# Optimization experiments

Hardware: AMD Instinct MI355X
Metric: run time of the kernel (lower is better)

## Reference

```python
import jax, jax.numpy as jnp
import numpy as np


def _conv(x, w, b, s):
    # x: NCHW, w: OIHW, VALID padding, stride s
    y = jax.lax.conv_general_dilated(x, w, (s, s), 'VALID',
                                     dimension_numbers=('NCHW', 'OIHW', 'NCHW'))
    return y + b[None, :, None, None]


def _deconv(x, w, b, s):
    # PyTorch ConvTranspose2d (weight IOHW, padding=0): conv of input dilated by s
    # with spatially-flipped, in/out-swapped kernel and full padding k-1.
    k = w.shape[2]
    wk = jnp.flip(w, (2, 3)).transpose(1, 0, 2, 3)  # -> OIHW
    y = jax.lax.conv_general_dilated(x, wk, (1, 1), [(k - 1, k - 1), (k - 1, k - 1)],
                                     lhs_dilation=(s, s),
                                     dimension_numbers=('NCHW', 'OIHW', 'NCHW'))
    return y + b[None, :, None, None]


def setup_inputs() -> dict:
    key = jax.random.key(0)
    ks = iter(jax.random.split(key, 40))
    def p(shape, scale=0.05):
        return jax.random.normal(next(ks), shape, jnp.float32) * scale
    return dict(
        x=jax.random.normal(next(ks), (50, 1, 64, 64), jnp.float32),
        action=jax.random.normal(next(ks), (50, 30), jnp.float32),
        h0=jax.random.normal(next(ks), (50, 1024), jnp.float32),
        c0=jax.random.normal(next(ks), (50, 1024), jnp.float32),
        conv1_w=p((32, 1, 4, 4)), conv1_b=p((32,)),
        conv2_w=p((64, 32, 4, 4)), conv2_b=p((64,)),
        conv3_w=p((128, 64, 4, 4)), conv3_b=p((128,)),
        conv4_w=p((256, 128, 4, 4)), conv4_b=p((256,)),
        fc1_w=p((482, 1024)), fc1_b=p((482,)),
        fc2_w=p((1024, 512)), fc2_b=p((1024,)),
        w_ih=p((4096, 1024)), w_hh=p((4096, 1024)),
        b_ih=p((4096,)), b_hh=p((4096,)),
        fcsd_w=p((1024, 1024)), fcsd_b=p((1024,)),
        d1_w=p((1024, 128, 5, 5)), d1_b=p((128,)),
        d2_w=p((128, 64, 5, 5)), d2_b=p((64,)),
        d3_w=p((64, 32, 6, 6)), d3_b=p((32,)),
        d4_w=p((32, 1, 6, 6)), d4_b=p((1,)),
        fc5_w=p((1, 512)), fc5_b=p((1,)),
    )


def reference(x, action, h0, c0,
              conv1_w, conv1_b, conv2_w, conv2_b, conv3_w, conv3_b, conv4_w, conv4_b,
              fc1_w, fc1_b, fc2_w, fc2_b,
              w_ih, w_hh, b_ih, b_hh,
              fcsd_w, fcsd_b,
              d1_w, d1_b, d2_w, d2_b, d3_w, d3_b, d4_w, d4_b,
              fc5_w, fc5_b):
    B = x.shape[0]  # 50 (hardcoded in original)
    T = 17          # PHYRE_MAX_TIMESTEPS
    h = x
    for w, b in ((conv1_w, conv1_b), (conv2_w, conv2_b), (conv3_w, conv3_b), (conv4_w, conv4_b)):
        h = jnp.tanh(_conv(h, w, b, 2))
    flat = h.reshape(B, -1)                      # [50, 1024]
    fc1 = flat @ fc1_w.T + fc1_b                 # [50, 482]
    z = jnp.concatenate([fc1, action], axis=1)   # [50, 512]
    fc2_out = jax.nn.leaky_relu(z @ fc2_w.T + fc2_b)  # [50, 1024]

    def step(carry, _):
        xt, hs, cs = carry
        g = xt @ w_ih.T + b_ih + hs @ w_hh.T + b_hh   # [B, 4096], gates i,f,g,o
        i, f, gg, o = jnp.split(g, 4, axis=1)
        cs = jax.nn.sigmoid(f) * cs + jax.nn.sigmoid(i) * jnp.tanh(gg)
        hs = jax.nn.sigmoid(o) * jnp.tanh(cs)
        return (hs, hs, cs), hs  # output fed back as next input

    _, outs = jax.lax.scan(step, (fc2_out, h0, c0), None, length=T)  # [17, 50, 1024]
    hd = jax.nn.leaky_relu(jnp.einsum('tbd,ed->tbe', outs, fcsd_w) + fcsd_b)
    hd = hd.reshape(T * B, 1024, 1, 1)  # t-major flatten, matching torch .view
    y = jnp.tanh(_deconv(hd, d1_w, d1_b, 2))   # [850,128,5,5]
    y = jnp.tanh(_deconv(y, d2_w, d2_b, 2))    # [850,64,13,13]
    y = jnp.tanh(_deconv(y, d3_w, d3_b, 2))    # [850,32,30,30]
    y = _deconv(y, d4_w, d4_b, 2)              # [850,1,64,64]
    obs = y.reshape(B, T, 1, 64, 64)  # faithful to original's view (layout quirk)
    reward = z @ fc5_w.T + fc5_b      # [50, 1]
    return obs, reward
```

## Files before the change

kernel.cpp:

```cpp
#include <hip/hip_runtime.h>
#include <math.h>

#define DI __device__ __forceinline__

DI float sigm(float x){ return 1.0f/(1.0f+expf(-x)); }
DI float lrelu(float x){ return x > 0.f ? x : 0.01f*x; }

template<int ACT>
DI float act_apply(float v){
    if (ACT == 1) return tanhf(v);
    if (ACT == 2) return lrelu(v);
    return v;
}

template<int CIN, int COUT>
__global__ __launch_bounds__(256)
void conv_enc_kernel(const float* __restrict__ in, const float* __restrict__ w,
                     const float* __restrict__ bias, float* __restrict__ out,
                     int N, int H, int OH)
{
    int idx = blockIdx.x*256 + threadIdx.x;
    int total = N*COUT*OH*OH;
    if (idx >= total) return;
    int ox = idx % OH; int t = idx / OH;
    int oy = t % OH;   t /= OH;
    int o  = t % COUT; int n = t / COUT;
    float acc = bias[o];
    const float* wp = w + o*CIN*16;
    const float* ip = in + ((size_t)n*CIN)*H*H + (oy*2)*H + ox*2;
    for (int c = 0; c < CIN; ++c) {
        const float* ipc = ip + c*H*H;
        const float* wpc = wp + c*16;
        #pragma unroll
        for (int ky = 0; ky < 4; ++ky)
            #pragma unroll
            for (int kx = 0; kx < 4; ++kx)
                acc += ipc[ky*H + kx] * wpc[ky*4 + kx];
    }
    out[idx] = tanhf(acc);
}

template<int BM,int BN,int BK,bool BT,int ACT>
__global__ __launch_bounds__((BM/4)*(BN/4))
void gemm_kernel(const float* __restrict__ A, const float* __restrict__ Bm,
                 const float* __restrict__ bias, float* __restrict__ C,
                 int M, int N, int Kfull, int klen, int ldc, int bias_div,
                 long partStride)
{
    constexpr int TM = 4, TN = 4;
    constexpr int THREADS = (BM/TM)*(BN/TN);
    constexpr int LDA = BM + 4, LDB = BN + 4;
    __shared__ __align__(16) float As[BK][LDA];
    __shared__ __align__(16) float Bs[BK][LDB];
    int tid = threadIdx.x;
    int m0 = blockIdx.y * BM, n0 = blockIdx.x * BN;
    int koff = blockIdx.z * klen;
    C += (long)blockIdx.z * partStride;
    constexpr int NTX = BN/TN;
    int tx = tid % NTX, ty = tid / NTX;
    float acc[4][4];
    #pragma unroll
    for (int i=0;i<4;++i)
        #pragma unroll
        for (int j=0;j<4;++j) acc[i][j] = 0.f;

    for (int k0 = 0; k0 < klen; k0 += BK) {
        for (int e = tid; e < BM*BK; e += THREADS) {
            int k = e % BK, m = e / BK;
            As[k][m] = (m0+m < M) ? A[(size_t)(m0+m)*Kfull + koff + k0 + k] : 0.f;
        }
        if (BT) {
            for (int e = tid; e < BN*BK; e += THREADS) {
                int k = e % BK, n = e / BK;
                Bs[k][n] = (n0+n < N) ? Bm[(size_t)(n0+n)*Kfull + koff + k0 + k] : 0.f;
            }
        } else {
            for (int e = tid; e < BN*BK; e += THREADS) {
                int n = e % BN, k = e / BN;
                Bs[k][n] = (n0+n < N) ? Bm[(size_t)(koff + k0 + k)*N + n0+n] : 0.f;
            }
        }
        __syncthreads();
        #pragma unroll 8
        for (int k = 0; k < BK; ++k) {
            float4 a4 = *reinterpret_cast<const float4*>(&As[k][ty*4]);
            float4 b4 = *reinterpret_cast<const float4*>(&Bs[k][tx*4]);
            float av[4] = {a4.x, a4.y, a4.z, a4.w};
            float bv[4] = {b4.x, b4.y, b4.z, b4.w};
            #pragma unroll
            for (int i=0;i<4;++i)
                #pragma unroll
                for (int j=0;j<4;++j)
                    acc[i][j] += av[i]*bv[j];
        }
        __syncthreads();
    }
    #pragma unroll
    for (int i=0;i<4;++i) {
        int m = m0 + ty*4 + i;
        if (m >= M) continue;
        #pragma unroll
        for (int j=0;j<4;++j) {
            int n = n0 + tx*4 + j;
            if (n >= N) continue;
            float v = acc[i][j] + (bias ? bias[n / bias_div] : 0.f);
            C[(size_t)m*ldc + n] = act_apply<ACT>(v);
        }
    }
}

__global__ __launch_bounds__(256)
void addvec_kernel(const float* __restrict__ a, const float* __restrict__ b,
                   float* __restrict__ o, int n)
{
    int i = blockIdx.x*256 + threadIdx.x;
    if (i < n) o[i] = a[i] + b[i];
}

__global__ __launch_bounds__(64)
void concat_action_kernel(const float* __restrict__ action, float* __restrict__ z)
{
    int i = blockIdx.x*64 + threadIdx.x;
    if (i < 50*30) { int b = i/30, k = i%30; z[b*512 + 482 + k] = action[i]; }
}

__global__ __launch_bounds__(64)
void reward_kernel(const float* __restrict__ z, const float* __restrict__ w,
                   const float* __restrict__ b, float* __restrict__ out)
{
    int bi = threadIdx.x;
    if (bi < 50) {
        float acc = b[0];
        for (int k = 0; k < 512; ++k) acc += z[bi*512 + k] * w[k];
        out[bi] = acc;
    }
}

__global__ __launch_bounds__(256)
void lstm_gates16_kernel(const float* __restrict__ gp, const float* __restrict__ bsum,
                         const float* __restrict__ c_prev,
                         float* __restrict__ c_out, float* __restrict__ h_out,
                         float* __restrict__ outs_t)
{
    int idx = blockIdx.x*256 + threadIdx.x;
    if (idx >= 50*1024) return;
    int b = idx >> 10, j = idx & 1023;
    float s0 = bsum[j], s1 = bsum[1024+j], s2 = bsum[2048+j], s3 = bsum[3072+j];
    #pragma unroll
    for (int p = 0; p < 16; ++p) {
        const float* base = gp + (size_t)p*204800 + b*4096 + j;
        s0 += base[0]; s1 += base[1024]; s2 += base[2048]; s3 += base[3072];
    }
    float cp = c_prev[idx];
    float c = sigm(s1)*cp + sigm(s0)*tanhf(s2);
    float h = sigm(s3)*tanhf(c);
    c_out[idx] = c; h_out[idx] = h; outs_t[idx] = h;
}

__global__ __launch_bounds__(256)
void wprep_kernel(const float* __restrict__ w, float* __restrict__ wp,
                  int CIN, int COUT, int KS)
{
    int idx = blockIdx.x*256 + threadIdx.x;
    int total = 4*CIN*COUT*12;
    if (idx >= total) return;
    int slot = idx % 12; int rem = idx / 12;
    int o = rem % COUT; rem /= COUT;
    int c = rem % CIN;  int pp = rem / CIN;
    int py = pp >> 1, px = pp & 1;
    int j = slot >> 2, i = slot & 3;
    int ky = py + 2*j, kx = px + 2*i;
    float v = 0.f;
    if (i < 3 && ky < KS && kx < KS)
        v = w[(((size_t)c*COUT + o)*KS + ky)*KS + kx];
    wp[idx] = v;
}

template<int CIN,int COUT,int HIN,int HOUT,int ACT,int CCHUNK,int ROWP,int TWU,int TB>
__global__ __launch_bounds__(256)
void deconv3_kernel(const float* __restrict__ in, const float* __restrict__ wp,
                    const float* __restrict__ bias, float* __restrict__ out, int N)
{
    constexpr int NCHUNK = CIN / CCHUNK;
    constexpr int NV = (HOUT + 1) / 2;
    constexpr int NTASK = COUT * NV * TB;
    constexpr int NR4 = (TWU + 2 + 3) / 4;
    static_assert(NCHUNK == 1 || NTASK <= 256, "multi-chunk needs <=1 task/thread");
    __shared__ __align__(16) float slab[CCHUNK*HIN*ROWP];
    int n = blockIdx.x;
    int tid = threadIdx.x;
    const float* inb = in + (size_t)n*CIN*HIN*HIN;
    const size_t PPSTR = (size_t)CIN*COUT*12;

    auto load_slab = [&](int c0){
        for (int r = tid; r < CCHUNK*HIN; r += 256) {
            int c = r / HIN, iy = r % HIN;
            const float* src = inb + ((size_t)(c0+c)*HIN + iy)*HIN;
            float* dst = slab + (c*HIN + iy)*ROWP;
            dst[0] = 0.f; dst[1] = 0.f;
            #pragma unroll
            for (int x2 = HIN+2; x2 < ROWP; ++x2) dst[x2] = 0.f;
            for (int x2 = 0; x2 < HIN; ++x2) dst[2+x2] = src[x2];
        }
    };

    auto chan_acc = [&](int cSlab, int cGlob, int o, int v, int u0,
                        float acc[2][2][TWU]) {
        const float* wbase = wp + ((size_t)cGlob*COUT + o)*12;
        const float* sc = slab + cSlab*(HIN*ROWP);
        #pragma unroll
        for (int jj = 0; jj < 3; ++jj) {
            int iy = v - jj;
            float r[NR4*4];
            if (iy >= 0 && iy < HIN) {
                const float* srow = sc + iy*ROWP + u0;
                #pragma unroll
                for (int q = 0; q < NR4; ++q) {
                    float4 f = *reinterpret_cast<const float4*>(srow + q*4);
                    r[q*4]=f.x; r[q*4+1]=f.y; r[q*4+2]=f.z; r[q*4+3]=f.w;
                }
            } else {
                #pragma unroll
                for (int q = 0; q < NR4*4; ++q) r[q] = 0.f;
            }
            #pragma unroll
            for (int pp = 0; pp < 4; ++pp) {
                float4 w4 = *reinterpret_cast<const float4*>(wbase + pp*PPSTR + jj*4);
                int py = pp >> 1, px = pp & 1;
                #pragma unroll
                for (int t = 0; t < TWU; ++t)
                    acc[py][px][t] += w4.x*r[t+2] + w4.y*r[t+1] + w4.z*r[t];
            }
        }
    };

    auto store_task = [&](int o, int v, int u0, float acc[2][2][TWU]) {
        float bv = bias[o];
        #pragma unroll
        for (int py = 0; py < 2; ++py) {
            int y = py + 2*v;
            if (y >= HOUT) continue;
            float* ob = out + (((size_t)n*COUT + o)*HOUT + y)*HOUT + 2*u0;
            #pragma unroll
            for (int t = 0; t < TWU; ++t) {
                int x0 = 2*(u0+t);
                if (x0 + 1 < HOUT) {
                    float2 q;
                    q.x = act_apply<ACT>(acc[py][0][t] + bv);
                    q.y = act_apply<ACT>(acc[py][1][t] + bv);
                    *reinterpret_cast<float2*>(ob + 2*t) = q;
                } else if (x0 < HOUT) {
                    ob[2*t] = act_apply<ACT>(acc[py][0][t] + bv);
                }
            }
        }
    };

    if constexpr (NCHUNK == 1) {
        load_slab(0);
        __syncthreads();
        for (int task = tid; task < NTASK; task += 256) {
            int v = task % NV; int rem = task / NV;
            int o = rem % COUT; int txb = rem / COUT;
            int u0 = txb * TWU;
            float acc[2][2][TWU];
            #pragma unroll
            for (int a=0;a<2;++a)
                #pragma unroll
                for (int b=0;b<2;++b)
                    #pragma unroll
                    for (int t=0;t<TWU;++t) acc[a][b][t] = 0.f;
            for (int c = 0; c < CIN; ++c)
                chan_acc(c, c, o, v, u0, acc);
            store_task(o, v, u0, acc);
        }
    } else {
        int task = tid;
        int v = task % NV; int rem = task / NV;
        int o = rem % COUT; int txb = rem / COUT;
        int u0 = txb * TWU;
        bool alive = (task < NTASK);
        float acc[2][2][TWU];
        #pragma unroll
        for (int a=0;a<2;++a)
            #pragma unroll
            for (int b=0;b<2;++b)
                #pragma unroll
                for (int t=0;t<TWU;++t) acc[a][b][t] = 0.f;
        for (int ch = 0; ch < NCHUNK; ++ch) {
            if (ch) __syncthreads();
            load_slab(ch*CCHUNK);
            __syncthreads();
            if (alive)
                for (int c = 0; c < CCHUNK; ++c)
                    chan_acc(c, ch*CCHUNK + c, o, v, u0, acc);
        }
        if (alive) store_task(o, v, u0, acc);
    }
}

extern "C" void kernel_launch(void* const* d_in, const int* in_sizes, int n_in,
                              void* d_out, int out_size, void* d_ws, size_t ws_size,
                              hipStream_t stream)
{
    const float* x       = (const float*)d_in[0];
    const float* action  = (const float*)d_in[1];
    const float* h0      = (const float*)d_in[2];
    const float* c0      = (const float*)d_in[3];
    const float* conv1_w = (const float*)d_in[4];  const float* conv1_b = (const float*)d_in[5];
    const float* conv2_w = (const float*)d_in[6];  const float* conv2_b = (const float*)d_in[7];
    const float* conv3_w = (const float*)d_in[8];  const float* conv3_b = (const float*)d_in[9];
    const float* conv4_w = (const float*)d_in[10]; const float* conv4_b = (const float*)d_in[11];
    const float* fc1_w   = (const float*)d_in[12]; const float* fc1_b   = (const float*)d_in[13];
    const float* fc2_w   = (const float*)d_in[14]; const float* fc2_b   = (const float*)d_in[15];
    const float* w_ih    = (const float*)d_in[16]; const float* w_hh    = (const float*)d_in[17];
    const float* b_ih    = (const float*)d_in[18]; const float* b_hh    = (const float*)d_in[19];
    const float* fcsd_w  = (const float*)d_in[20]; const float* fcsd_b  = (const float*)d_in[21];
    const float* d1_w    = (const float*)d_in[22]; const float* d1_b    = (const float*)d_in[23];
    const float* d2_w    = (const float*)d_in[24]; const float* d2_b    = (const float*)d_in[25];
    const float* d3_w    = (const float*)d_in[26]; const float* d3_b    = (const float*)d_in[27];
    const float* d4_w    = (const float*)d_in[28]; const float* d4_b    = (const float*)d_in[29];
    const float* fc5_w   = (const float*)d_in[30]; const float* fc5_b   = (const float*)d_in[31];
    float* out = (float*)d_out;
    float* ws  = (float*)d_ws;

    float* a1   = ws;
    float* a2   = a1 + 1537600;
    float* a3   = a2 + 627200;
    float* flat = a3 + 230400;
    float* z    = flat + 51200;
    float* fc2o = z + 25600;
    float* hbuf = fc2o + 51200;
    float* cbuf = hbuf + 51200;
    float* outs = cbuf + 51200;
    float* hd   = outs + 870400;
    float* wsum = hd + 870400;
    float* bsum = wsum + 4194304;
    float* wp2  = bsum + 4096;
    float* wp3  = wp2 + 393216;
    float* wp4  = wp3 + 98304;
    float* y1   = wp4 + 1536;
    float* y2   = y1 + 2720000;
    float* y3   = y2 + 9193600;
    float* g16  = y1;

    const int B = 50;
    const long GP = 204800;

    addvec_kernel<<<(4194304+255)/256, 256, 0, stream>>>(w_ih, w_hh, wsum, 4194304);
    addvec_kernel<<<(4096+255)/256, 256, 0, stream>>>(b_ih, b_hh, bsum, 4096);
    wprep_kernel<<<(4*128*64*12+255)/256, 256, 0, stream>>>(d2_w, wp2, 128, 64, 5);
    wprep_kernel<<<(4*64*32*12+255)/256, 256, 0, stream>>>(d3_w, wp3, 64, 32, 6);
    wprep_kernel<<<(4*32*1*12+255)/256, 256, 0, stream>>>(d4_w, wp4, 32, 1, 6);

    conv_enc_kernel<1,32><<<(B*32*31*31+255)/256, 256, 0, stream>>>(x, conv1_w, conv1_b, a1, B, 64, 31);
    conv_enc_kernel<32,64><<<(B*64*14*14+255)/256, 256, 0, stream>>>(a1, conv2_w, conv2_b, a2, B, 31, 14);
    conv_enc_kernel<64,128><<<(B*128*6*6+255)/256, 256, 0, stream>>>(a2, conv3_w, conv3_b, a3, B, 14, 6);
    conv_enc_kernel<128,256><<<(B*256*2*2+255)/256, 256, 0, stream>>>(a3, conv4_w, conv4_b, flat, B, 6, 2);

    {
        dim3 grid((482+63)/64, (B+31)/32, 1);
        gemm_kernel<32,64,32,true,0><<<grid, 128, 0, stream>>>(flat, fc1_w, fc1_b, z, B, 482, 1024, 1024, 512, 1, 0);
    }
    concat_action_kernel<<<(1500+63)/64, 64, 0, stream>>>(action, z);
    reward_kernel<<<1, 64, 0, stream>>>(z, fc5_w, fc5_b, out + (size_t)850*4096);

    {
        dim3 grid((1024+63)/64, (B+31)/32, 1);
        gemm_kernel<32,64,32,true,2><<<grid, 128, 0, stream>>>(z, fc2_w, fc2_b, fc2o, B, 1024, 512, 512, 1024, 1, 0);
    }

    {
        dim3 grid0(64, 2, 8);
        gemm_kernel<32,64,32,true,0><<<grid0, 128, 0, stream>>>(fc2o, w_ih, nullptr, g16, B, 4096, 1024, 128, 4096, 1, GP);
        gemm_kernel<32,64,32,true,0><<<grid0, 128, 0, stream>>>(h0, w_hh, nullptr, g16 + 8*GP, B, 4096, 1024, 128, 4096, 1, GP);
        lstm_gates16_kernel<<<200, 256, 0, stream>>>(g16, bsum, c0, cbuf, hbuf, outs);
        dim3 gridt(64, 2, 16);
        for (int t = 1; t < 17; ++t) {
            gemm_kernel<32,64,32,true,0><<<gridt, 128, 0, stream>>>(hbuf, wsum, nullptr, g16, B, 4096, 1024, 64, 4096, 1, GP);
            lstm_gates16_kernel<<<200, 256, 0, stream>>>(g16, bsum, cbuf, cbuf, hbuf, outs + (size_t)t*51200);
        }
    }

    {
        dim3 grid((1024+63)/64, (850+63)/64, 1);
        gemm_kernel<64,64,32,true,2><<<grid, 256, 0, stream>>>(outs, fcsd_w, fcsd_b, hd, 850, 1024, 1024, 1024, 1024, 1, 0);
    }
    {
        dim3 grid((3200+63)/64, (850+63)/64, 1);
        gemm_kernel<64,64,32,false,1><<<grid, 256, 0, stream>>>(hd, d1_w, d1_b, y1, 850, 3200, 1024, 1024, 3200, 25, 0);
    }
    deconv3_kernel<128,64,5,13,1, 128,12,7,1><<<850, 256, 0, stream>>>(y1, wp2, d2_b, y2, 850);
    deconv3_kernel<64,32,13,30,1, 64,20,15,1><<<850, 256, 0, stream>>>(y2, wp3, d3_b, y3, 850);
    deconv3_kernel<32,1,30,64,0, 16,36,4,8><<<850, 256, 0, stream>>>(y3, wp4, d4_b, out, 850);

    (void)in_sizes; (void)n_in; (void)out_size; (void)ws_size;
}
```

Before: 3.194 ms.

## Split transposed-conv kernels across row segments with multi-row register tiling

Replaces the deconv3 kernel with deconv4. The new kernel splits each sample's output rows across several blocks (VSPLIT) and loads only the input rows each segment needs into shared memory. It can compute several output rows per thread (VPER) for register reuse of weights, and it sets a minimum-waves launch bound. The layer configurations change: d3 now runs on 1700 blocks, and d4 runs on 3400 blocks with one column per thread instead of chunked channels. Explicit fmaf is also used in the GEMM and conv loops. The aim is more parallelism and better occupancy in the dominant deconv stages, at the cost of redundant halo-row loads and more register pressure.

```diff
diff --git a/kernel.cpp b/kernel.cpp
--- a/kernel.cpp
+++ b/kernel.cpp
@@ -35,7 +35,7 @@
         for (int ky = 0; ky < 4; ++ky)
             #pragma unroll
             for (int kx = 0; kx < 4; ++kx)
-                acc += ipc[ky*H + kx] * wpc[ky*4 + kx];
+                acc = fmaf(ipc[ky*H + kx], wpc[ky*4 + kx], acc);
     }
     out[idx] = tanhf(acc);
 }
@@ -91,7 +91,7 @@
             for (int i=0;i<4;++i)
                 #pragma unroll
                 for (int j=0;j<4;++j)
-                    acc[i][j] += av[i]*bv[j];
+                    acc[i][j] = fmaf(av[i], bv[j], acc[i][j]);
         }
         __syncthreads();
     }
@@ -131,7 +131,7 @@
     int bi = threadIdx.x;
     if (bi < 50) {
         float acc = b[0];
-        for (int k = 0; k < 512; ++k) acc += z[bi*512 + k] * w[k];
+        for (int k = 0; k < 512; ++k) acc = fmaf(z[bi*512 + k], w[k], acc);
         out[bi] = acc;
     }
 }
@@ -176,126 +176,133 @@
     wp[idx] = v;
 }
 
-template<int CIN,int COUT,int HIN,int HOUT,int ACT,int CCHUNK,int ROWP,int TWU,int TB>
-__global__ __launch_bounds__(256)
-void deconv3_kernel(const float* __restrict__ in, const float* __restrict__ wp,
-                    const float* __restrict__ bias, float* __restrict__ out, int N)
-{
-    constexpr int NCHUNK = CIN / CCHUNK;
+template<int CIN,int COUT,int HIN,int HOUT,int ACT,int VSPLIT,int ROWP,int TWU,
+         int VPER,int TB,int MWAVES>
+__global__ __launch_bounds__(256, MWAVES)
+void deconv4_kernel(const float* __restrict__ in, const float* __restrict__ wp,
+                    const float* __restrict__ bias, float* __restrict__ out)
+{
     constexpr int NV = (HOUT + 1) / 2;
-    constexpr int NTASK = COUT * NV * TB;
+    constexpr int NVSEG = (NV + VSPLIT - 1) / VSPLIT;
+    constexpr int NVB = (NVSEG + VPER - 1) / VPER;
+    constexpr int ROWS_MAX = NVSEG + 2;
     constexpr int NR4 = (TWU + 2 + 3) / 4;
-    static_assert(NCHUNK == 1 || NTASK <= 256, "multi-chunk needs <=1 task/thread");
-    __shared__ __align__(16) float slab[CCHUNK*HIN*ROWP];
-    int n = blockIdx.x;
+    constexpr int RLEN = (TWU == 1) ? 4 : NR4*4;
+    static_assert(NVB * COUT * TB <= 256, "tasks must fit one per thread");
+    __shared__ __align__(16) float slab[CIN*ROWS_MAX*ROWP];
+
+    int n   = blockIdx.x / VSPLIT;
+    int seg = blockIdx.x % VSPLIT;
+    int v0 = seg * NVSEG;
+    int v1 = (v0 + NVSEG < NV) ? v0 + NVSEG : NV;
+    int r0 = (v0 - 2 > 0) ? v0 - 2 : 0;
+    int r1m = (v1 - 1 < HIN - 1) ? v1 - 1 : HIN - 1;
+    int nrows = r1m - r0 + 1;
     int tid = threadIdx.x;
     const float* inb = in + (size_t)n*CIN*HIN*HIN;
     const size_t PPSTR = (size_t)CIN*COUT*12;
 
-    auto load_slab = [&](int c0){
-        for (int r = tid; r < CCHUNK*HIN; r += 256) {
-            int c = r / HIN, iy = r % HIN;
-            const float* src = inb + ((size_t)(c0+c)*HIN + iy)*HIN;
-            float* dst = slab + (c*HIN + iy)*ROWP;
+    for (int e = tid; e < CIN*ROWS_MAX; e += 256) {
+        int c = e / ROWS_MAX, ri = e % ROWS_MAX;
+        if (ri < nrows) {
+            const float* src = inb + ((size_t)c*HIN + r0 + ri)*HIN;
+            float* dst = slab + (c*ROWS_MAX + ri)*ROWP;
             dst[0] = 0.f; dst[1] = 0.f;
             #pragma unroll
             for (int x2 = HIN+2; x2 < ROWP; ++x2) dst[x2] = 0.f;
             for (int x2 = 0; x2 < HIN; ++x2) dst[2+x2] = src[x2];
         }
-    };
-
-    auto chan_acc = [&](int cSlab, int cGlob, int o, int v, int u0,
-                        float acc[2][2][TWU]) {
-        const float* wbase = wp + ((size_t)cGlob*COUT + o)*12;
-        const float* sc = slab + cSlab*(HIN*ROWP);
+    }
+    __syncthreads();
+
+    int task = tid;
+    int vi = task % NVB; int rem = task / NVB;
+    int o = rem % COUT;  int tb = rem / COUT;
+    int u0 = tb * TWU;
+    bool anyv = false;
+    int vg[VPER];
+    #pragma unroll
+    for (int q = 0; q < VPER; ++q) {
+        vg[q] = v0 + vi + q*NVB;
+        if (vg[q] < v1) anyv = true;
+    }
+    if (tb >= TB) anyv = false;
+
+    float acc[VPER][2][2][TWU];
+    #pragma unroll
+    for (int q=0;q<VPER;++q)
         #pragma unroll
-        for (int jj = 0; jj < 3; ++jj) {
-            int iy = v - jj;
-            float r[NR4*4];
-            if (iy >= 0 && iy < HIN) {
-                const float* srow = sc + iy*ROWP + u0;
+        for (int a=0;a<2;++a)
+            #pragma unroll
+            for (int b=0;b<2;++b)
                 #pragma unroll
-                for (int q = 0; q < NR4; ++q) {
-                    float4 f = *reinterpret_cast<const float4*>(srow + q*4);
-                    r[q*4]=f.x; r[q*4+1]=f.y; r[q*4+2]=f.z; r[q*4+3]=f.w;
+                for (int t=0;t<TWU;++t) acc[q][a][b][t] = 0.f;
+
+    if (anyv) {
+        const float* wb0 = wp + ((size_t)0*COUT + o)*12;
+        for (int c = 0; c < CIN; ++c) {
+            const float* wbase = wb0 + (size_t)c*COUT*12;
+            const float* sc = slab + c*(ROWS_MAX*ROWP);
+            #pragma unroll
+            for (int jj = 0; jj < 3; ++jj) {
+                float r[VPER][RLEN];
+                #pragma unroll
+                for (int q = 0; q < VPER; ++q) {
+                    int iy = vg[q] - jj;
+                    if (iy >= 0 && iy < HIN) {
+                        const float* srow = sc + (iy - r0)*ROWP + u0;
+                        if constexpr (TWU == 1) {
+                            r[q][0] = srow[0]; r[q][1] = srow[1]; r[q][2] = srow[2];
+                        } else {
+                            #pragma unroll
+                            for (int p4 = 0; p4 < NR4; ++p4) {
+                                float4 f = *reinterpret_cast<const float4*>(srow + p4*4);
+                                r[q][p4*4]=f.x; r[q][p4*4+1]=f.y; r[q][p4*4+2]=f.z; r[q][p4*4+3]=f.w;
+                            }
+                        }
+                    } else {
+                        #pragma unroll
+                        for (int p4 = 0; p4 < RLEN; ++p4) r[q][p4] = 0.f;
+                    }
                 }
-            } else {
                 #pragma unroll
-                for (int q = 0; q < NR4*4; ++q) r[q] = 0.f;
+                for (int pp = 0; pp < 4; ++pp) {
+                    float4 w4 = *reinterpret_cast<const float4*>(wbase + pp*PPSTR + jj*4);
+                    int py = pp >> 1, px = pp & 1;
+                    #pragma unroll
+                    for (int q = 0; q < VPER; ++q)
+                        #pragma unroll
+                        for (int t = 0; t < TWU; ++t)
+                            acc[q][py][px][t] =
+                                fmaf(w4.x, r[q][t+2],
+                                fmaf(w4.y, r[q][t+1],
+                                fmaf(w4.z, r[q][t], acc[q][py][px][t])));
+                }
             }
-            #pragma unroll
-            for (int pp = 0; pp < 4; ++pp) {
-                float4 w4 = *reinterpret_cast<const float4*>(wbase + pp*PPSTR + jj*4);
-                int py = pp >> 1, px = pp & 1;
-                #pragma unroll
-                for (int t = 0; t < TWU; ++t)
-                    acc[py][px][t] += w4.x*r[t+2] + w4.y*r[t+1] + w4.z*r[t];
-            }
-        }
-    };
-
-    auto store_task = [&](int o, int v, int u0, float acc[2][2][TWU]) {
+        }
         float bv = bias[o];
         #pragma unroll
-        for (int py = 0; py < 2; ++py) {
-            int y = py + 2*v;
-            if (y >= HOUT) continue;
-            float* ob = out + (((size_t)n*COUT + o)*HOUT + y)*HOUT + 2*u0;
-            #pragma unroll
-            for (int t = 0; t < TWU; ++t) {
-                int x0 = 2*(u0+t);
-                if (x0 + 1 < HOUT) {
-                    float2 q;
-                    q.x = act_apply<ACT>(acc[py][0][t] + bv);
-                    q.y = act_apply<ACT>(acc[py][1][t] + bv);
-                    *reinterpret_cast<float2*>(ob + 2*t) = q;
-                } else if (x0 < HOUT) {
-                    ob[2*t] = act_apply<ACT>(acc[py][0][t] + bv);
+        for (int q = 0; q < VPER; ++q) {
+            if (vg[q] >= v1) continue;
+            #pragma unroll
+            for (int py = 0; py < 2; ++py) {
+                int y = py + 2*vg[q];
+                if (y >= HOUT) continue;
+                float* ob = out + (((size_t)n*COUT + o)*HOUT + y)*HOUT;
+                #pragma unroll
+                for (int t = 0; t < TWU; ++t) {
+                    int x0 = 2*(u0+t);
+                    if (x0 + 1 < HOUT) {
+                        float2 qv;
+                        qv.x = act_apply<ACT>(acc[q][py][0][t] + bv);
+                        qv.y = act_apply<ACT>(acc[q][py][1][t] + bv);
+                        *reinterpret_cast<float2*>(ob + x0) = qv;
+                    } else if (x0 < HOUT) {
+                        ob[x0] = act_apply<ACT>(acc[q][py][0][t] + bv);
+                    }
                 }
             }
         }
-    };
-
-    if constexpr (NCHUNK == 1) {
-        load_slab(0);
-        __syncthreads();
-        for (int task = tid; task < NTASK; task += 256) {
-            int v = task % NV; int rem = task / NV;
-            int o = rem % COUT; int txb = rem / COUT;
-            int u0 = txb * TWU;
-            float acc[2][2][TWU];
-            #pragma unroll
-            for (int a=0;a<2;++a)
-                #pragma unroll
-                for (int b=0;b<2;++b)
-                    #pragma unroll
-                    for (int t=0;t<TWU;++t) acc[a][b][t] = 0.f;
-            for (int c = 0; c < CIN; ++c)
-                chan_acc(c, c, o, v, u0, acc);
-            store_task(o, v, u0, acc);
-        }
-    } else {
-        int task = tid;
-        int v = task % NV; int rem = task / NV;
-        int o = rem % COUT; int txb = rem / COUT;
-        int u0 = txb * TWU;
-        bool alive = (task < NTASK);
-        float acc[2][2][TWU];
-        #pragma unroll
-        for (int a=0;a<2;++a)
-            #pragma unroll
-            for (int b=0;b<2;++b)
-                #pragma unroll
-                for (int t=0;t<TWU;++t) acc[a][b][t] = 0.f;
-        for (int ch = 0; ch < NCHUNK; ++ch) {
-            if (ch) __syncthreads();
-            load_slab(ch*CCHUNK);
-            __syncthreads();
-            if (alive)
-                for (int c = 0; c < CCHUNK; ++c)
-                    chan_acc(c, ch*CCHUNK + c, o, v, u0, acc);
-        }
-        if (alive) store_task(o, v, u0, acc);
     }
 }
 
@@ -390,9 +397,10 @@
         dim3 grid((3200+63)/64, (850+63)/64, 1);
         gemm_kernel<64,64,32,false,1><<<grid, 256, 0, stream>>>(hd, d1_w, d1_b, y1, 850, 3200, 1024, 1024, 3200, 25, 0);
     }
-    deconv3_kernel<128,64,5,13,1, 128,12,7,1><<<850, 256, 0, stream>>>(y1, wp2, d2_b, y2, 850);
-    deconv3_kernel<64,32,13,30,1, 64,20,15,1><<<850, 256, 0, stream>>>(y2, wp3, d3_b, y3, 850);
-    deconv3_kernel<32,1,30,64,0, 16,36,4,8><<<850, 256, 0, stream>>>(y3, wp4, d4_b, out, 850);
+
+    deconv4_kernel<128,64,5,13,1, 1,12,7,2,1,4><<<850, 256, 0, stream>>>(y1, wp2, d2_b, y2);
+    deconv4_kernel<64,32,13,30,1, 2,20,15,1,1,3><<<1700, 256, 0, stream>>>(y2, wp3, d3_b, y3);
+    deconv4_kernel<32,1,30,64,0, 4,36,1,1,32,3><<<3400, 256, 0, stream>>>(y3, wp4, d4_b, out);
 
     (void)in_sizes; (void)n_in; (void)out_size; (void)ws_size;
 }
```

Result: faster. 3.035 ms (-5.0%).
